# Kernel tuning notes

Hardware: AMD Instinct MI355X
Metric: run time of the kernel (lower is better)

## Reference

```python
import jax, jax.numpy as jnp
import numpy as np

N_NODES = 50000
N_EDGES = 800000
NFEAT, NHID, NCLASS = 512, 128, 40
PN_SCALE = 1.0


def spmm(edge_row, edge_col, edge_val, h):
    # sparse [N,N] @ dense [N,F]: out[r] += val * h[c] for each edge (r, c)
    msgs = edge_val[:, None] * h[edge_col]  # [E, F]
    return jax.ops.segment_sum(msgs, edge_row, num_segments=N_NODES)


def pair_norm(x):
    # mode 'PN': center columns, scale by mean row norm
    x = x - x.mean(axis=0)
    rownorm_mean = jnp.sqrt(1e-6 + (x * x).sum(axis=1).mean())
    return PN_SCALE * x / rownorm_mean


def setup_inputs() -> dict:
    key = jax.random.key(0)
    ks = jax.random.split(key, 12)

    def uinit(k, shape, fan_out):
        stdv = 1.0 / np.sqrt(fan_out)
        return jax.random.uniform(k, shape, jnp.float32, -stdv, stdv)

    return {
        "x": jax.random.normal(ks[0], (N_NODES, NFEAT), jnp.float32),
        "edge_row": jax.random.randint(ks[1], (N_EDGES,), 0, N_NODES),
        "edge_col": jax.random.randint(ks[2], (N_EDGES,), 0, N_NODES),
        "edge_val": jax.random.uniform(ks[3], (N_EDGES,), jnp.float32),
        "W0": uinit(ks[4], (NFEAT, NHID), NHID),
        "b0": uinit(ks[5], (1, NHID), NHID),
        "W1": uinit(ks[6], (NHID, NHID), NHID),
        "b1": uinit(ks[7], (1, NHID), NHID),
        "W2": uinit(ks[8], (NHID, NHID), NHID),
        "b2": uinit(ks[9], (1, NHID), NHID),
        "W_out": uinit(ks[10], (NHID, NCLASS), NCLASS),
        "b_out": uinit(ks[11], (1, NCLASS), NCLASS),
    }


def reference(x, edge_row, edge_col, edge_val,
              W0, b0, W1, b1, W2, b2, W_out, b_out):
    # DeepGCN forward, eval mode (dropout p=0 is identity), residual=1 -> skip every layer
    x_old = 0.0
    for W, b in ((W0, b0), (W1, b1), (W2, b2)):
        h = x @ W                             # dense mm
        h = spmm(edge_row, edge_col, edge_val, h) + b  # sparse aggregate + bias
        h = pair_norm(h)
        h = jax.nn.relu(h)
        h = h + x_old                         # residual (x_old=0 on first layer)
        x_old = h
        x = h
    out = spmm(edge_row, edge_col, edge_val, x @ W_out) + b_out
    return out
```

## Files before the change

### kernel.cpp

```cpp
#include <hip/hip_runtime.h>
#include <hip/hip_bf16.h>
#include <math.h>

#define N_NODES 50000
#define N_EDGES 800000
#define NFEAT   512
#define NHID    128
#define NCLASS  40
#define NB_STATS 256
#define NPASS    8
#define ROWS_PER_PASS (N_NODES / NPASS)
#define SCAN_BLOCKS ((N_NODES + 1023) / 1024)

typedef short bf16x8 __attribute__((ext_vector_type(8)));
typedef float f32x4  __attribute__((ext_vector_type(4)));

__device__ inline float bf2f(unsigned short u) {
    union { unsigned int i; float f; } x; x.i = ((unsigned int)u) << 16; return x.f;
}

__global__ void hist_kernel(const int* __restrict__ rows, int* __restrict__ cnt, int n) {
    int i = blockIdx.x * blockDim.x + threadIdx.x;
    if (i < n) atomicAdd(&cnt[rows[i]], 1);
}

__global__ __launch_bounds__(1024) void scan_p1_kernel(const int* __restrict__ cnt,
                                                       int* __restrict__ bsum, int n) {
    int i = blockIdx.x * 1024 + threadIdx.x;
    int v = (i < n) ? cnt[i] : 0;
    __shared__ int sm[16];
    int lane = threadIdx.x & 63, w = threadIdx.x >> 6;
    #pragma unroll
    for (int off = 32; off > 0; off >>= 1) v += __shfl_xor(v, off, 64);
    if (lane == 0) sm[w] = v;
    __syncthreads();
    if (threadIdx.x == 0) {
        int s = 0;
        #pragma unroll
        for (int j = 0; j < 16; ++j) s += sm[j];
        bsum[blockIdx.x] = s;
    }
}

__global__ void scan_p2_kernel(int* __restrict__ bsum, int nb) {
    int t = threadIdx.x;
    int v = (t < nb) ? bsum[t] : 0;
    int x = v;
    #pragma unroll
    for (int off = 1; off < 64; off <<= 1) {
        int y = __shfl_up(x, off, 64);
        if (t >= off) x += y;
    }
    if (t < nb) bsum[t] = x - v;
}

__global__ __launch_bounds__(1024) void scan_p3_kernel(const int* __restrict__ cnt,
                                                       const int* __restrict__ bsum,
                                                       int* __restrict__ row_ptr,
                                                       int* __restrict__ cursor, int n) {
    __shared__ int wsum[16];
    int b = blockIdx.x;
    int i = b * 1024 + threadIdx.x;
    int lane = threadIdx.x & 63, w = threadIdx.x >> 6;
    int v = (i < n) ? cnt[i] : 0;
    int x = v;
    #pragma unroll
    for (int off = 1; off < 64; off <<= 1) {
        int y = __shfl_up(x, off, 64);
        if (lane >= off) x += y;
    }
    if (lane == 63) wsum[w] = x;
    __syncthreads();
    int wbase = 0;
    for (int j = 0; j < w; ++j) wbase += wsum[j];
    int incl = bsum[b] + wbase + x;
    if (i < n) {
        row_ptr[i + 1] = incl;
        cursor[i] = incl - v;
    }
    if (i == 0) row_ptr[0] = 0;
}

__global__ void scatter_kernel(const int* __restrict__ rows, const int* __restrict__ cols,
                               const float* __restrict__ vals, int* __restrict__ cursor,
                               int2* __restrict__ csr_cv, int n, int blocksPerPass) {
    int p = blockIdx.x / blocksPerPass;
    int b = blockIdx.x % blocksPerPass;
    int i = b * 256 + threadIdx.x;
    if (i >= n) return;
    int r = rows[i];
    int lo = p * ROWS_PER_PASS;
    if (r < lo || r >= lo + ROWS_PER_PASS) return;
    int pos = atomicAdd(&cursor[r], 1);
    csr_cv[pos] = make_int2(cols[i], __float_as_int(vals[i]));
}

__global__ __launch_bounds__(256) void wt_cvt_all_kernel(const float* __restrict__ W0,
        const float* __restrict__ W1, const float* __restrict__ W2,
        const float* __restrict__ Wo, __hip_bfloat16* __restrict__ Wt0,
        __hip_bfloat16* __restrict__ Wt1, __hip_bfloat16* __restrict__ Wt2,
        __hip_bfloat16* __restrict__ Wot) {
    int i = blockIdx.x * blockDim.x + threadIdx.x;
    if (i < 65536) {
        int k = i >> 7, n = i & 127;
        Wt0[(size_t)n * 512 + k] = __float2bfloat16(W0[i]);
    } else if (i < 65536 + 16384) {
        int j = i - 65536; int k = j >> 7, n = j & 127;
        Wt1[(size_t)n * 128 + k] = __float2bfloat16(W1[j]);
    } else if (i < 65536 + 32768) {
        int j = i - 65536 - 16384; int k = j >> 7, n = j & 127;
        Wt2[(size_t)n * 128 + k] = __float2bfloat16(W2[j]);
    } else if (i < 65536 + 32768 + 8192) {
        int j = i - 65536 - 32768; int k = j >> 6, n = j & 63;
        float v = (n < NCLASS) ? Wo[k * NCLASS + n] : 0.f;
        Wot[(size_t)n * 128 + k] = __float2bfloat16(v);
    }
}

template<int BM, int BN, int K>
__global__ __launch_bounds__(256) void mfma_gemm(const __hip_bfloat16* __restrict__ Xb,
                                                 const __hip_bfloat16* __restrict__ Wt,
                                                 __hip_bfloat16* __restrict__ Ob, int M) {
    constexpr int BK  = 64;
    constexpr int LDK = 72;
    constexpr int WN  = BN / 64;
    __shared__ short As[BM * LDK];
    __shared__ short Bs[BN * LDK];
    int t = threadIdx.x;
    int lane = t & 63;
    int w = t >> 6;
    int wm = w / WN, wn = w % WN;
    int row0 = blockIdx.x * BM;
    int m0 = wm * 32, n0 = wn * 64;
    int l15 = lane & 15, quad = lane >> 4;

    f32x4 acc[2][4] = {};

    for (int k0 = 0; k0 < K; k0 += BK) {
        #pragma unroll
        for (int idx = t; idx < BM * 8; idx += 256) {
            int r = idx >> 3, c = idx & 7;
            uint4 v = make_uint4(0u, 0u, 0u, 0u);
            if (row0 + r < M)
                v = *(const uint4*)(Xb + (size_t)(row0 + r) * K + k0 + c * 8);
            *(uint4*)(As + r * LDK + c * 8) = v;
        }
        #pragma unroll
        for (int idx = t; idx < BN * 8; idx += 256) {
            int r = idx >> 3, c = idx & 7;
            uint4 v = *(const uint4*)(Wt + (size_t)r * K + k0 + c * 8);
            *(uint4*)(Bs + r * LDK + c * 8) = v;
        }
        __syncthreads();
        #pragma unroll
        for (int ks = 0; ks < 2; ++ks) {
            bf16x8 af[2], bfv[4];
            #pragma unroll
            for (int mt = 0; mt < 2; ++mt)
                af[mt] = *(const bf16x8*)(As + (m0 + mt * 16 + l15) * LDK + ks * 32 + quad * 8);
            #pragma unroll
            for (int nt = 0; nt < 4; ++nt)
                bfv[nt] = *(const bf16x8*)(Bs + (n0 + nt * 16 + l15) * LDK + ks * 32 + quad * 8);
            #pragma unroll
            for (int mt = 0; mt < 2; ++mt)
                #pragma unroll
                for (int nt = 0; nt < 4; ++nt)
                    acc[mt][nt] = __builtin_amdgcn_mfma_f32_16x16x32_bf16(
                        af[mt], bfv[nt], acc[mt][nt], 0, 0, 0);
        }
        __syncthreads();
    }
    #pragma unroll
    for (int mt = 0; mt < 2; ++mt) {
        #pragma unroll
        for (int reg = 0; reg < 4; ++reg) {
            int row = row0 + m0 + mt * 16 + quad * 4 + reg;
            if (row < M) {
                #pragma unroll
                for (int nt = 0; nt < 4; ++nt)
                    Ob[(size_t)row * BN + n0 + nt * 16 + l15] =
                        __float2bfloat16(acc[mt][nt][reg]);
            }
        }
    }
}

template<int BM, int BN, int K>
__global__ __launch_bounds__(256) void mfma_gemm_f32a(const float* __restrict__ Xg,
                                                      const __hip_bfloat16* __restrict__ Wt,
                                                      __hip_bfloat16* __restrict__ Ob, int M) {
    constexpr int BK  = 64;
    constexpr int LDK = 72;
    constexpr int WN  = BN / 64;
    __shared__ short As[BM * LDK];
    __shared__ short Bs[BN * LDK];
    int t = threadIdx.x;
    int lane = t & 63;
    int w = t >> 6;
    int wm = w / WN, wn = w % WN;
    int row0 = blockIdx.x * BM;
    int m0 = wm * 32, n0 = wn * 64;
    int l15 = lane & 15, quad = lane >> 4;

    f32x4 acc[2][4] = {};

    for (int k0 = 0; k0 < K; k0 += BK) {
        #pragma unroll
        for (int idx = t; idx < BM * 16; idx += 256) {
            int r = idx >> 4, c = idx & 15;
            float4 v = make_float4(0.f, 0.f, 0.f, 0.f);
            if (row0 + r < M)
                v = *(const float4*)(Xg + (size_t)(row0 + r) * K + k0 + c * 4);
            __hip_bfloat16 o[4] = {__float2bfloat16(v.x), __float2bfloat16(v.y),
                                   __float2bfloat16(v.z), __float2bfloat16(v.w)};
            *(short4*)(As + r * LDK + c * 4) = *(short4*)o;
        }
        #pragma unroll
        for (int idx = t; idx < BN * 8; idx += 256) {
            int r = idx >> 3, c = idx & 7;
            uint4 v = *(const uint4*)(Wt + (size_t)r * K + k0 + c * 8);
            *(uint4*)(Bs + r * LDK + c * 8) = v;
        }
        __syncthreads();
        #pragma unroll
        for (int ks = 0; ks < 2; ++ks) {
            bf16x8 af[2], bfv[4];
            #pragma unroll
            for (int mt = 0; mt < 2; ++mt)
                af[mt] = *(const bf16x8*)(As + (m0 + mt * 16 + l15) * LDK + ks * 32 + quad * 8);
            #pragma unroll
            for (int nt = 0; nt < 4; ++nt)
                bfv[nt] = *(const bf16x8*)(Bs + (n0 + nt * 16 + l15) * LDK + ks * 32 + quad * 8);
            #pragma unroll
            for (int mt = 0; mt < 2; ++mt)
                #pragma unroll
                for (int nt = 0; nt < 4; ++nt)
                    acc[mt][nt] = __builtin_amdgcn_mfma_f32_16x16x32_bf16(
                        af[mt], bfv[nt], acc[mt][nt], 0, 0, 0);
        }
        __syncthreads();
    }
    #pragma unroll
    for (int mt = 0; mt < 2; ++mt) {
        #pragma unroll
        for (int reg = 0; reg < 4; ++reg) {
            int row = row0 + m0 + mt * 16 + quad * 4 + reg;
            if (row < M) {
                #pragma unroll
                for (int nt = 0; nt < 4; ++nt)
                    Ob[(size_t)row * BN + n0 + nt * 16 + l15] =
                        __float2bfloat16(acc[mt][nt][reg]);
            }
        }
    }
}

__global__ __launch_bounds__(256) void spmm_bf16_kernel(const __hip_bfloat16* __restrict__ H,
                                                        const int* __restrict__ row_ptr,
                                                        const int2* __restrict__ cv,
                                                        const float* __restrict__ bias,
                                                        __hip_bfloat16* __restrict__ Bm,
                                                        int nrows) {
    int wid = (int)((blockIdx.x * blockDim.x + threadIdx.x) >> 6);
    wid = __builtin_amdgcn_readfirstlane(wid);
    int lane = threadIdx.x & 63;
    int h = lane >> 5;
    int sub = lane & 31;
    if (wid >= nrows) return;
    int s = row_ptr[wid];
    int e = row_ptr[wid + 1];
    const ushort4* H4 = (const ushort4*)H;
    f32x4 acc = {0.f, 0.f, 0.f, 0.f};
    int i = s;
    for (; i + 3 < e; i += 4) {
        int2 c0 = cv[i], c1 = cv[i + 1], c2 = cv[i + 2], c3 = cv[i + 3];
        int   ca = h ? c2.x : c0.x;
        float va = __int_as_float(h ? c2.y : c0.y);
        int   cb = h ? c3.x : c1.x;
        float vb = __int_as_float(h ? c3.y : c1.y);
        ushort4 ga = H4[(size_t)ca * 32 + sub];
        ushort4 gb = H4[(size_t)cb * 32 + sub];
        acc[0] = fmaf(va, bf2f(ga.x), acc[0]); acc[1] = fmaf(va, bf2f(ga.y), acc[1]);
        acc[2] = fmaf(va, bf2f(ga.z), acc[2]); acc[3] = fmaf(va, bf2f(ga.w), acc[3]);
        acc[0] = fmaf(vb, bf2f(gb.x), acc[0]); acc[1] = fmaf(vb, bf2f(gb.y), acc[1]);
        acc[2] = fmaf(vb, bf2f(gb.z), acc[2]); acc[3] = fmaf(vb, bf2f(gb.w), acc[3]);
    }
    for (; i < e; ++i) {
        int2 c = cv[i];
        if (h == 0) {
            float v = __int_as_float(c.y);
            ushort4 g = H4[(size_t)c.x * 32 + sub];
            acc[0] = fmaf(v, bf2f(g.x), acc[0]); acc[1] = fmaf(v, bf2f(g.y), acc[1]);
            acc[2] = fmaf(v, bf2f(g.z), acc[2]); acc[3] = fmaf(v, bf2f(g.w), acc[3]);
        }
    }
    #pragma unroll
    for (int c = 0; c < 4; ++c) acc[c] += __shfl_xor(acc[c], 32);
    if (h == 0) {
        float4 b4 = *(const float4*)(bias + 4 * sub);
        __hip_bfloat16 o[4] = {__float2bfloat16(acc[0] + b4.x), __float2bfloat16(acc[1] + b4.y),
                               __float2bfloat16(acc[2] + b4.z), __float2bfloat16(acc[3] + b4.w)};
        *(ushort4*)(Bm + (size_t)wid * 128 + 4 * sub) = *(ushort4*)o;
    }
}

__global__ __launch_bounds__(256) void stats_kernel(const __hip_bfloat16* __restrict__ B,
                                                    float* __restrict__ partials, int n2) {
    int tid = blockIdx.x * blockDim.x + threadIdx.x;
    int stride = NB_STATS * 256;
    const __hip_bfloat162* B2 = (const __hip_bfloat162*)B;
    float cs0 = 0.f, cs1 = 0.f, sq = 0.f;
    for (int j = tid; j < n2; j += stride) {
        __hip_bfloat162 h = B2[j];
        float a = __bfloat162float(h.x), b = __bfloat162float(h.y);
        cs0 += a; cs1 += b;
        sq = fmaf(a, a, sq); sq = fmaf(b, b, sq);
    }
    __shared__ float s0[256], s1[256], ss[256];
    int t = threadIdx.x;
    s0[t] = cs0; s1[t] = cs1; ss[t] = sq;
    __syncthreads();
    if (t < 64) {
        float a = s0[t] + s0[t + 64] + s0[t + 128] + s0[t + 192];
        float b = s1[t] + s1[t + 64] + s1[t + 128] + s1[t + 192];
        float* pb = partials + (size_t)blockIdx.x * 132;
        pb[2 * t] = a;
        pb[2 * t + 1] = b;
    }
    __syncthreads();
    for (int off = 128; off > 0; off >>= 1) {
        if (t < off) ss[t] += ss[t + off];
        __syncthreads();
    }
    if (t == 0) partials[(size_t)blockIdx.x * 132 + 128] = ss[0];
}

__global__ void finalize_stats_kernel(const float* __restrict__ partials,
                                      float* __restrict__ stats, int nrows) {
    int t = threadIdx.x;
    float cs = 0.f;
    for (int b = 0; b < NB_STATS; ++b) cs += partials[(size_t)b * 132 + t];
    float mu = cs / (float)nrows;
    __shared__ float smu2[128];
    __shared__ float ssq[128];
    float sq = 0.f;
    for (int b = t; b < NB_STATS; b += 128) sq += partials[(size_t)b * 132 + 128];
    smu2[t] = mu * mu;
    ssq[t] = sq;
    __syncthreads();
    for (int off = 64; off > 0; off >>= 1) {
        if (t < off) { smu2[t] += smu2[t + off]; ssq[t] += ssq[t + off]; }
        __syncthreads();
    }
    if (t == 0) {
        float ms = ssq[0] / (float)nrows - smu2[0];
        stats[129] = 1.0f / sqrtf(1e-6f + ms);
    }
    stats[t] = mu;
}

__global__ __launch_bounds__(256) void pn_apply_kernel(const __hip_bfloat16* __restrict__ B,
                                                       const float* __restrict__ stats,
                                                       __hip_bfloat16* __restrict__ Xb,
                                                       int n4, int addResid) {
    int i = blockIdx.x * blockDim.x + threadIdx.x;
    if (i >= n4) return;
    ushort4 bv = *(const ushort4*)(B + (size_t)i * 4);
    __hip_bfloat16* bb = (__hip_bfloat16*)&bv;
    int c4 = (i << 2) & 127;
    float s = stats[129];
    float4 m = ((const float4*)stats)[c4 >> 2];
    float r0 = 0.f, r1 = 0.f, r2 = 0.f, r3 = 0.f;
    if (addResid) {
        ushort4 rv = *(const ushort4*)(Xb + (size_t)i * 4);
        __hip_bfloat16* rb = (__hip_bfloat16*)&rv;
        r0 = __bfloat162float(rb[0]); r1 = __bfloat162float(rb[1]);
        r2 = __bfloat162float(rb[2]); r3 = __bfloat162float(rb[3]);
    }
    __hip_bfloat16 o[4];
    o[0] = __float2bfloat16(fmaxf((__bfloat162float(bb[0]) - m.x) * s, 0.f) + r0);
    o[1] = __float2bfloat16(fmaxf((__bfloat162float(bb[1]) - m.y) * s, 0.f) + r1);
    o[2] = __float2bfloat16(fmaxf((__bfloat162float(bb[2]) - m.z) * s, 0.f) + r2);
    o[3] = __float2bfloat16(fmaxf((__bfloat162float(bb[3]) - m.w) * s, 0.f) + r3);
    *(ushort4*)(Xb + (size_t)i * 4) = *(ushort4*)o;
}

__global__ __launch_bounds__(256) void spmm_out_kernel(const __hip_bfloat16* __restrict__ G,
                                                       const int* __restrict__ row_ptr,
                                                       const int2* __restrict__ cv,
                                                       const float* __restrict__ bias,
                                                       float* __restrict__ out, int nrows) {
    int wid = (int)((blockIdx.x * blockDim.x + threadIdx.x) >> 6);
    wid = __builtin_amdgcn_readfirstlane(wid);
    int lane = threadIdx.x & 63;
    int h = lane >> 5;
    int sub = lane & 31;
    if (wid >= nrows) return;
    int s = row_ptr[wid];
    int e = row_ptr[wid + 1];
    const __hip_bfloat162* G2 = (const __hip_bfloat162*)G;
    float a0 = 0.f, a1 = 0.f;
    int i = s;
    for (; i + 3 < e; i += 4) {
        int2 c0 = cv[i], c1 = cv[i + 1], c2 = cv[i + 2], c3 = cv[i + 3];
        int   ca = h ? c2.x : c0.x;
        float va = __int_as_float(h ? c2.y : c0.y);
        int   cb = h ? c3.x : c1.x;
        float vb = __int_as_float(h ? c3.y : c1.y);
        __hip_bfloat162 ga = G2[(size_t)ca * 32 + sub];
        __hip_bfloat162 gb = G2[(size_t)cb * 32 + sub];
        a0 = fmaf(va, __bfloat162float(ga.x), a0); a1 = fmaf(va, __bfloat162float(ga.y), a1);
        a0 = fmaf(vb, __bfloat162float(gb.x), a0); a1 = fmaf(vb, __bfloat162float(gb.y), a1);
    }
    for (; i < e; ++i) {
        int2 c = cv[i];
        if (h == 0) {
            float v = __int_as_float(c.y);
            __hip_bfloat162 g = G2[(size_t)c.x * 32 + sub];
            a0 = fmaf(v, __bfloat162float(g.x), a0);
            a1 = fmaf(v, __bfloat162float(g.y), a1);
        }
    }
    a0 += __shfl_xor(a0, 32);
    a1 += __shfl_xor(a1, 32);
    if (h == 0 && sub < NCLASS / 2) {
        float2 b2 = *(const float2*)(bias + 2 * sub);
        float2 o = make_float2(a0 + b2.x, a1 + b2.y);
        *(float2*)(out + (size_t)wid * NCLASS + 2 * sub) = o;
    }
}

extern "C" void kernel_launch(void* const* d_in, const int* in_sizes, int n_in,
                              void* d_out, int out_size, void* d_ws, size_t ws_size,
                              hipStream_t stream) {
    const float* x        = (const float*)d_in[0];
    const int*   edge_row = (const int*)  d_in[1];
    const int*   edge_col = (const int*)  d_in[2];
    const float* edge_val = (const float*)d_in[3];
    const float* W0 = (const float*)d_in[4];
    const float* b0 = (const float*)d_in[5];
    const float* W1 = (const float*)d_in[6];
    const float* b1 = (const float*)d_in[7];
    const float* W2 = (const float*)d_in[8];
    const float* b2 = (const float*)d_in[9];
    const float* W_out = (const float*)d_in[10];
    const float* b_out = (const float*)d_in[11];
    float* out = (float*)d_out;

    const size_t NH = (size_t)N_NODES * NHID;

    char* p = (char*)d_ws;
    __hip_bfloat16* Xb   = (__hip_bfloat16*)p;  p += NH * 2;
    __hip_bfloat16* A_bf = (__hip_bfloat16*)p;  p += NH * 2;
    __hip_bfloat16* Bm   = (__hip_bfloat16*)p;  p += NH * 2;
    __hip_bfloat16* Wt0 = (__hip_bfloat16*)p;   p += (size_t)128 * 512 * 2;
    __hip_bfloat16* Wt1 = (__hip_bfloat16*)p;   p += (size_t)128 * 128 * 2;
    __hip_bfloat16* Wt2 = (__hip_bfloat16*)p;   p += (size_t)128 * 128 * 2;
    __hip_bfloat16* Wot = (__hip_bfloat16*)p;   p += (size_t)64 * 128 * 2;
    float* stats    = (float*)p;                p += 132 * 4;
    float* partials = (float*)p;                p += (size_t)NB_STATS * 132 * 4;
    int* cnt      = (int*)p;                    p += (size_t)N_NODES * 4;
    int* row_ptr  = (int*)p;                    p += (size_t)(N_NODES + 1) * 4 + 4;
    int* cursor   = (int*)p;                    p += (size_t)N_NODES * 4;
    int* bsum     = (int*)p;                    p += (size_t)SCAN_BLOCKS * 4 + 4;
    int2* csr_cv  = (int2*)p;                   p += (size_t)N_EDGES * 8;

    const int EB = (N_EDGES + 255) / 256;
    const int SPMM_GRID = (N_NODES + 3) / 4;
    const int PN_GRID = (int)(NH / 4 + 255) / 256;

    wt_cvt_all_kernel<<<(65536 + 32768 + 8192 + 255) / 256, 256, 0, stream>>>(
        W0, W1, W2, W_out, Wt0, Wt1, Wt2, Wot);

    hipMemsetAsync(cnt, 0, N_NODES * sizeof(int), stream);
    hist_kernel<<<EB, 256, 0, stream>>>(edge_row, cnt, N_EDGES);
    scan_p1_kernel<<<SCAN_BLOCKS, 1024, 0, stream>>>(cnt, bsum, N_NODES);
    scan_p2_kernel<<<1, 64, 0, stream>>>(bsum, SCAN_BLOCKS);
    scan_p3_kernel<<<SCAN_BLOCKS, 1024, 0, stream>>>(cnt, bsum, row_ptr, cursor, N_NODES);
    scatter_kernel<<<EB * NPASS, 256, 0, stream>>>(edge_row, edge_col, edge_val, cursor,
                                                   csr_cv, N_EDGES, EB);

    mfma_gemm_f32a<64, 128, 512><<<(N_NODES + 63) / 64, 256, 0, stream>>>(x, Wt0, A_bf, N_NODES);
    spmm_bf16_kernel<<<SPMM_GRID, 256, 0, stream>>>(A_bf, row_ptr, csr_cv, b0, Bm, N_NODES);
    stats_kernel<<<NB_STATS, 256, 0, stream>>>(Bm, partials, (int)(NH / 2));
    finalize_stats_kernel<<<1, 128, 0, stream>>>(partials, stats, N_NODES);
    pn_apply_kernel<<<PN_GRID, 256, 0, stream>>>(Bm, stats, Xb, (int)(NH / 4), 0);

    const __hip_bfloat16* Wts[2] = {Wt1, Wt2};
    const float* bs[2] = {b1, b2};
    for (int l = 0; l < 2; ++l) {
        mfma_gemm<64, 128, 128><<<(N_NODES + 63) / 64, 256, 0, stream>>>(Xb, Wts[l], A_bf, N_NODES);
        spmm_bf16_kernel<<<SPMM_GRID, 256, 0, stream>>>(A_bf, row_ptr, csr_cv, bs[l], Bm, N_NODES);
        stats_kernel<<<NB_STATS, 256, 0, stream>>>(Bm, partials, (int)(NH / 2));
        finalize_stats_kernel<<<1, 128, 0, stream>>>(partials, stats, N_NODES);
        pn_apply_kernel<<<PN_GRID, 256, 0, stream>>>(Bm, stats, Xb, (int)(NH / 4), 1);
    }

    mfma_gemm<128, 64, 128><<<(N_NODES + 127) / 128, 256, 0, stream>>>(Xb, Wot, A_bf, N_NODES);
    spmm_out_kernel<<<SPMM_GRID, 256, 0, stream>>>(A_bf, row_ptr, csr_cv, b_out,
                                                   out, N_NODES);
}
```

Measured before the change: 521.8 us.

## Bucket CSR edges by column range within rows and unroll SpMM gathers by eight

The CSR build now counts and scatters edges per (row, column-bucket) pair, so each row's neighbors are ordered by one of eight column ranges. The intent is to improve cache locality of the feature-row gathers in the sparse aggregation. The histogram, scan and cursor arrays grow eightfold, and the block-sum scan becomes multi-wave. The SpMM kernels also gain an 8-edge unrolled loop to issue more independent gathers per iteration.

```diff
diff --git a/kernel.cpp b/kernel.cpp
--- a/kernel.cpp
+++ b/kernel.cpp
@@ -10,7 +10,10 @@
 #define NB_STATS 256
 #define NPASS    8
 #define ROWS_PER_PASS (N_NODES / NPASS)
-#define SCAN_BLOCKS ((N_NODES + 1023) / 1024)
+#define NCB      8
+#define CB_W     (N_NODES / NCB)
+#define NCNT     (N_NODES * NCB)
+#define SCAN_BLOCKS ((NCNT + 1023) / 1024)
 
 typedef short bf16x8 __attribute__((ext_vector_type(8)));
 typedef float f32x4  __attribute__((ext_vector_type(4)));
@@ -19,9 +22,14 @@
     union { unsigned int i; float f; } x; x.i = ((unsigned int)u) << 16; return x.f;
 }
 
-__global__ void hist_kernel(const int* __restrict__ rows, int* __restrict__ cnt, int n) {
+__global__ void hist_kernel(const int* __restrict__ rows, const int* __restrict__ cols,
+                            int* __restrict__ cnt, int n) {
     int i = blockIdx.x * blockDim.x + threadIdx.x;
-    if (i < n) atomicAdd(&cnt[rows[i]], 1);
+    if (i < n) {
+        int r = rows[i];
+        int cb = cols[i] / CB_W;
+        atomicAdd(&cnt[r * NCB + cb], 1);
+    }
 }
 
 __global__ __launch_bounds__(1024) void scan_p1_kernel(const int* __restrict__ cnt,
@@ -42,21 +50,27 @@
     }
 }
 
-__global__ void scan_p2_kernel(int* __restrict__ bsum, int nb) {
+__global__ __launch_bounds__(512) void scan_p2_kernel(int* __restrict__ bsum, int nb) {
+    __shared__ int wsum[8];
     int t = threadIdx.x;
+    int lane = t & 63, w = t >> 6;
     int v = (t < nb) ? bsum[t] : 0;
     int x = v;
     #pragma unroll
     for (int off = 1; off < 64; off <<= 1) {
         int y = __shfl_up(x, off, 64);
-        if (t >= off) x += y;
-    }
-    if (t < nb) bsum[t] = x - v;
+        if (lane >= off) x += y;
+    }
+    if (lane == 63) wsum[w] = x;
+    __syncthreads();
+    int wbase = 0;
+    for (int j = 0; j < w; ++j) wbase += wsum[j];
+    if (t < nb) bsum[t] = wbase + x - v;
 }
 
 __global__ __launch_bounds__(1024) void scan_p3_kernel(const int* __restrict__ cnt,
                                                        const int* __restrict__ bsum,
-                                                       int* __restrict__ row_ptr,
+                                                       int* __restrict__ bptr,
                                                        int* __restrict__ cursor, int n) {
     __shared__ int wsum[16];
     int b = blockIdx.x;
@@ -75,10 +89,10 @@
     for (int j = 0; j < w; ++j) wbase += wsum[j];
     int incl = bsum[b] + wbase + x;
     if (i < n) {
-        row_ptr[i + 1] = incl;
+        bptr[i + 1] = incl;
         cursor[i] = incl - v;
     }
-    if (i == 0) row_ptr[0] = 0;
+    if (i == 0) bptr[0] = 0;
 }
 
 __global__ void scatter_kernel(const int* __restrict__ rows, const int* __restrict__ cols,
@@ -91,8 +105,9 @@
     int r = rows[i];
     int lo = p * ROWS_PER_PASS;
     if (r < lo || r >= lo + ROWS_PER_PASS) return;
-    int pos = atomicAdd(&cursor[r], 1);
-    csr_cv[pos] = make_int2(cols[i], __float_as_int(vals[i]));
+    int c = cols[i];
+    int pos = atomicAdd(&cursor[r * NCB + c / CB_W], 1);
+    csr_cv[pos] = make_int2(c, __float_as_int(vals[i]));
 }
 
 __global__ __launch_bounds__(256) void wt_cvt_all_kernel(const float* __restrict__ W0,
@@ -256,7 +271,7 @@
 }
 
 __global__ __launch_bounds__(256) void spmm_bf16_kernel(const __hip_bfloat16* __restrict__ H,
-                                                        const int* __restrict__ row_ptr,
+                                                        const int* __restrict__ bptr,
                                                         const int2* __restrict__ cv,
                                                         const float* __restrict__ bias,
                                                         __hip_bfloat16* __restrict__ Bm,
@@ -267,19 +282,37 @@
     int h = lane >> 5;
     int sub = lane & 31;
     if (wid >= nrows) return;
-    int s = row_ptr[wid];
-    int e = row_ptr[wid + 1];
+    int s = bptr[wid * NCB];
+    int e = bptr[wid * NCB + NCB];
     const ushort4* H4 = (const ushort4*)H;
     f32x4 acc = {0.f, 0.f, 0.f, 0.f};
     int i = s;
+    for (; i + 7 < e; i += 8) {
+        int2 c0 = cv[i],     c1 = cv[i + 1], c2 = cv[i + 2], c3 = cv[i + 3];
+        int2 c4 = cv[i + 4], c5 = cv[i + 5], c6 = cv[i + 6], c7 = cv[i + 7];
+        int   ka = h ? c4.x : c0.x;  float va = __int_as_float(h ? c4.y : c0.y);
+        int   kb = h ? c5.x : c1.x;  float vb = __int_as_float(h ? c5.y : c1.y);
+        int   kc = h ? c6.x : c2.x;  float vc = __int_as_float(h ? c6.y : c2.y);
+        int   kd = h ? c7.x : c3.x;  float vd = __int_as_float(h ? c7.y : c3.y);
+        ushort4 ga = H4[(size_t)ka * 32 + sub];
+        ushort4 gb = H4[(size_t)kb * 32 + sub];
+        ushort4 gc = H4[(size_t)kc * 32 + sub];
+        ushort4 gd = H4[(size_t)kd * 32 + sub];
+        acc[0] = fmaf(va, bf2f(ga.x), acc[0]); acc[1] = fmaf(va, bf2f(ga.y), acc[1]);
+        acc[2] = fmaf(va, bf2f(ga.z), acc[2]); acc[3] = fmaf(va, bf2f(ga.w), acc[3]);
+        acc[0] = fmaf(vb, bf2f(gb.x), acc[0]); acc[1] = fmaf(vb, bf2f(gb.y), acc[1]);
+        acc[2] = fmaf(vb, bf2f(gb.z), acc[2]); acc[3] = fmaf(vb, bf2f(gb.w), acc[3]);
+        acc[0] = fmaf(vc, bf2f(gc.x), acc[0]); acc[1] = fmaf(vc, bf2f(gc.y), acc[1]);
+        acc[2] = fmaf(vc, bf2f(gc.z), acc[2]); acc[3] = fmaf(vc, bf2f(gc.w), acc[3]);
+        acc[0] = fmaf(vd, bf2f(gd.x), acc[0]); acc[1] = fmaf(vd, bf2f(gd.y), acc[1]);
+        acc[2] = fmaf(vd, bf2f(gd.z), acc[2]); acc[3] = fmaf(vd, bf2f(gd.w), acc[3]);
+    }
     for (; i + 3 < e; i += 4) {
         int2 c0 = cv[i], c1 = cv[i + 1], c2 = cv[i + 2], c3 = cv[i + 3];
-        int   ca = h ? c2.x : c0.x;
-        float va = __int_as_float(h ? c2.y : c0.y);
-        int   cb = h ? c3.x : c1.x;
-        float vb = __int_as_float(h ? c3.y : c1.y);
-        ushort4 ga = H4[(size_t)ca * 32 + sub];
-        ushort4 gb = H4[(size_t)cb * 32 + sub];
+        int   ka = h ? c2.x : c0.x;  float va = __int_as_float(h ? c2.y : c0.y);
+        int   kb = h ? c3.x : c1.x;  float vb = __int_as_float(h ? c3.y : c1.y);
+        ushort4 ga = H4[(size_t)ka * 32 + sub];
+        ushort4 gb = H4[(size_t)kb * 32 + sub];
         acc[0] = fmaf(va, bf2f(ga.x), acc[0]); acc[1] = fmaf(va, bf2f(ga.y), acc[1]);
         acc[2] = fmaf(va, bf2f(ga.z), acc[2]); acc[3] = fmaf(va, bf2f(ga.w), acc[3]);
         acc[0] = fmaf(vb, bf2f(gb.x), acc[0]); acc[1] = fmaf(vb, bf2f(gb.y), acc[1]);
@@ -386,7 +419,7 @@
 }
 
 __global__ __launch_bounds__(256) void spmm_out_kernel(const __hip_bfloat16* __restrict__ G,
-                                                       const int* __restrict__ row_ptr,
+                                                       const int* __restrict__ bptr,
                                                        const int2* __restrict__ cv,
                                                        const float* __restrict__ bias,
                                                        float* __restrict__ out, int nrows) {
@@ -396,19 +429,33 @@
     int h = lane >> 5;
     int sub = lane & 31;
     if (wid >= nrows) return;
-    int s = row_ptr[wid];
-    int e = row_ptr[wid + 1];
+    int s = bptr[wid * NCB];
+    int e = bptr[wid * NCB + NCB];
     const __hip_bfloat162* G2 = (const __hip_bfloat162*)G;
     float a0 = 0.f, a1 = 0.f;
     int i = s;
+    for (; i + 7 < e; i += 8) {
+        int2 c0 = cv[i],     c1 = cv[i + 1], c2 = cv[i + 2], c3 = cv[i + 3];
+        int2 c4 = cv[i + 4], c5 = cv[i + 5], c6 = cv[i + 6], c7 = cv[i + 7];
+        int   ka = h ? c4.x : c0.x;  float va = __int_as_float(h ? c4.y : c0.y);
+        int   kb = h ? c5.x : c1.x;  float vb = __int_as_float(h ? c5.y : c1.y);
+        int   kc = h ? c6.x : c2.x;  float vc = __int_as_float(h ? c6.y : c2.y);
+        int   kd = h ? c7.x : c3.x;  float vd = __int_as_float(h ? c7.y : c3.y);
+        __hip_bfloat162 ga = G2[(size_t)ka * 32 + sub];
+        __hip_bfloat162 gb = G2[(size_t)kb * 32 + sub];
+        __hip_bfloat162 gc = G2[(size_t)kc * 32 + sub];
+        __hip_bfloat162 gd = G2[(size_t)kd * 32 + sub];
+        a0 = fmaf(va, __bfloat162float(ga.x), a0); a1 = fmaf(va, __bfloat162float(ga.y), a1);
+        a0 = fmaf(vb, __bfloat162float(gb.x), a0); a1 = fmaf(vb, __bfloat162float(gb.y), a1);
+        a0 = fmaf(vc, __bfloat162float(gc.x), a0); a1 = fmaf(vc, __bfloat162float(gc.y), a1);
+        a0 = fmaf(vd, __bfloat162float(gd.x), a0); a1 = fmaf(vd, __bfloat162float(gd.y), a1);
+    }
     for (; i + 3 < e; i += 4) {
         int2 c0 = cv[i], c1 = cv[i + 1], c2 = cv[i + 2], c3 = cv[i + 3];
-        int   ca = h ? c2.x : c0.x;
-        float va = __int_as_float(h ? c2.y : c0.y);
-        int   cb = h ? c3.x : c1.x;
-        float vb = __int_as_float(h ? c3.y : c1.y);
-        __hip_bfloat162 ga = G2[(size_t)ca * 32 + sub];
-        __hip_bfloat162 gb = G2[(size_t)cb * 32 + sub];
+        int   ka = h ? c2.x : c0.x;  float va = __int_as_float(h ? c2.y : c0.y);
+        int   kb = h ? c3.x : c1.x;  float vb = __int_as_float(h ? c3.y : c1.y);
+        __hip_bfloat162 ga = G2[(size_t)ka * 32 + sub];
+        __hip_bfloat162 gb = G2[(size_t)kb * 32 + sub];
         a0 = fmaf(va, __bfloat162float(ga.x), a0); a1 = fmaf(va, __bfloat162float(ga.y), a1);
         a0 = fmaf(vb, __bfloat162float(gb.x), a0); a1 = fmaf(vb, __bfloat162float(gb.y), a1);
     }
@@ -459,9 +506,9 @@
     __hip_bfloat16* Wot = (__hip_bfloat16*)p;   p += (size_t)64 * 128 * 2;
     float* stats    = (float*)p;                p += 132 * 4;
     float* partials = (float*)p;                p += (size_t)NB_STATS * 132 * 4;
-    int* cnt      = (int*)p;                    p += (size_t)N_NODES * 4;
-    int* row_ptr  = (int*)p;                    p += (size_t)(N_NODES + 1) * 4 + 4;
-    int* cursor   = (int*)p;                    p += (size_t)N_NODES * 4;
+    int* cnt      = (int*)p;                    p += (size_t)NCNT * 4;
+    int* bptr     = (int*)p;                    p += (size_t)(NCNT + 1) * 4 + 4;
+    int* cursor   = (int*)p;                    p += (size_t)NCNT * 4;
     int* bsum     = (int*)p;                    p += (size_t)SCAN_BLOCKS * 4 + 4;
     int2* csr_cv  = (int2*)p;                   p += (size_t)N_EDGES * 8;
 
@@ -472,16 +519,16 @@
     wt_cvt_all_kernel<<<(65536 + 32768 + 8192 + 255) / 256, 256, 0, stream>>>(
         W0, W1, W2, W_out, Wt0, Wt1, Wt2, Wot);
 
-    hipMemsetAsync(cnt, 0, N_NODES * sizeof(int), stream);
-    hist_kernel<<<EB, 256, 0, stream>>>(edge_row, cnt, N_EDGES);
-    scan_p1_kernel<<<SCAN_BLOCKS, 1024, 0, stream>>>(cnt, bsum, N_NODES);
-    scan_p2_kernel<<<1, 64, 0, stream>>>(bsum, SCAN_BLOCKS);
-    scan_p3_kernel<<<SCAN_BLOCKS, 1024, 0, stream>>>(cnt, bsum, row_ptr, cursor, N_NODES);
+    hipMemsetAsync(cnt, 0, NCNT * sizeof(int), stream);
+    hist_kernel<<<EB, 256, 0, stream>>>(edge_row, edge_col, cnt, N_EDGES);
+    scan_p1_kernel<<<SCAN_BLOCKS, 1024, 0, stream>>>(cnt, bsum, NCNT);
+    scan_p2_kernel<<<1, 512, 0, stream>>>(bsum, SCAN_BLOCKS);
+    scan_p3_kernel<<<SCAN_BLOCKS, 1024, 0, stream>>>(cnt, bsum, bptr, cursor, NCNT);
     scatter_kernel<<<EB * NPASS, 256, 0, stream>>>(edge_row, edge_col, edge_val, cursor,
                                                    csr_cv, N_EDGES, EB);
 
     mfma_gemm_f32a<64, 128, 512><<<(N_NODES + 63) / 64, 256, 0, stream>>>(x, Wt0, A_bf, N_NODES);
-    spmm_bf16_kernel<<<SPMM_GRID, 256, 0, stream>>>(A_bf, row_ptr, csr_cv, b0, Bm, N_NODES);
+    spmm_bf16_kernel<<<SPMM_GRID, 256, 0, stream>>>(A_bf, bptr, csr_cv, b0, Bm, N_NODES);
     stats_kernel<<<NB_STATS, 256, 0, stream>>>(Bm, partials, (int)(NH / 2));
     finalize_stats_kernel<<<1, 128, 0, stream>>>(partials, stats, N_NODES);
     pn_apply_kernel<<<PN_GRID, 256, 0, stream>>>(Bm, stats, Xb, (int)(NH / 4), 0);
@@ -490,13 +537,13 @@
     const float* bs[2] = {b1, b2};
     for (int l = 0; l < 2; ++l) {
         mfma_gemm<64, 128, 128><<<(N_NODES + 63) / 64, 256, 0, stream>>>(Xb, Wts[l], A_bf, N_NODES);
-        spmm_bf16_kernel<<<SPMM_GRID, 256, 0, stream>>>(A_bf, row_ptr, csr_cv, bs[l], Bm, N_NODES);
+        spmm_bf16_kernel<<<SPMM_GRID, 256, 0, stream>>>(A_bf, bptr, csr_cv, bs[l], Bm, N_NODES);
         stats_kernel<<<NB_STATS, 256, 0, stream>>>(Bm, partials, (int)(NH / 2));
         finalize_stats_kernel<<<1, 128, 0, stream>>>(partials, stats, N_NODES);
         pn_apply_kernel<<<PN_GRID, 256, 0, stream>>>(Bm, stats, Xb, (int)(NH / 4), 1);
     }
 
     mfma_gemm<128, 64, 128><<<(N_NODES + 127) / 128, 256, 0, stream>>>(Xb, Wot, A_bf, N_NODES);
-    spmm_out_kernel<<<SPMM_GRID, 256, 0, stream>>>(A_bf, row_ptr, csr_cv, b_out,
+    spmm_out_kernel<<<SPMM_GRID, 256, 0, stream>>>(A_bf, bptr, csr_cv, b_out,
                                                    out, N_NODES);
 }
```

Measured after the change: 496.6 us. 4.8% less time.
